# Kernel tuning notes

Measured on AMD Instinct MI355X. Metric: run time of the kernel, lower is better.

## Reference

```python
import jax, jax.numpy as jnp
import numpy as np

WIN = 8          # window side
N = WIN * WIN    # tokens per window = 64
C = 180          # channels
H = 6            # heads
D = C // H       # head dim = 30


def _relative_index():
    coords = jnp.stack(jnp.meshgrid(jnp.arange(WIN), jnp.arange(WIN), indexing='ij'))
    coords = coords.reshape(2, -1)                       # (2, N)
    rel = coords[:, :, None] - coords[:, None, :]        # (2, N, N)
    idx = (rel[0] + WIN - 1) * (2 * WIN - 1) + (rel[1] + WIN - 1)
    return idx.reshape(-1)                               # (N*N,) int


def setup_inputs() -> dict:
    key = jax.random.key(0)
    ks = jax.random.split(key, 6)
    B, WNum = 4096, 1024
    windows = jax.random.normal(ks[0], (B, N, C), dtype=jnp.float32)
    mask = jax.random.normal(ks[1], (WNum, N, N), dtype=jnp.float32)
    w_qkv = jax.random.normal(ks[2], (C, 3 * C), dtype=jnp.float32) * 0.02
    bias_table = jax.random.normal(ks[3], ((2 * WIN - 1) ** 2, H), dtype=jnp.float32) * 0.02
    w_proj = jax.random.normal(ks[4], (C, C), dtype=jnp.float32) * 0.02
    b_proj = jnp.zeros((C,), dtype=jnp.float32)
    return {"windows": windows, "mask": mask, "w_qkv": w_qkv,
            "bias_table": bias_table, "w_proj": w_proj, "b_proj": b_proj}


def reference(windows, mask, w_qkv, bias_table, w_proj, b_proj):
    B, n, c = windows.shape
    WNum = mask.shape[0]
    rel_idx = _relative_index()

    # qkv projection: (B, N, 3C) -> (3, B, H, N, D)
    qkv = (windows @ w_qkv).reshape(B, n, 3, H, D).transpose(2, 0, 3, 1, 4)
    q, k, v = qkv[0], qkv[1], qkv[2]

    scale = 1.0 / jnp.sqrt(jnp.float32(D))
    scores = jnp.einsum('bhnd,bhmd->bhnm', q, k) * scale     # (B, H, N, N)

    # relative position bias gather: (N*N, H) -> (H, N, N)
    rel_bias = bias_table[rel_idx].reshape(n, n, H).transpose(2, 0, 1)
    scores = scores + rel_bias[None]

    # per-window mask add
    scores = scores.reshape(B // WNum, WNum, H, n, n) + mask[None, :, None, :, :]
    scores = scores.reshape(B, H, n, n)

    attn = jax.nn.softmax(scores, axis=-1)
    out = jnp.einsum('bhnm,bhmd->bhnd', attn, v)             # (B, H, N, D)
    z = out.transpose(0, 2, 1, 3).reshape(B, n, c)
    return z @ w_proj + b_proj
```

## Files before the change

### kernel.cpp

```cpp
#include <hip/hip_runtime.h>


typedef __bf16 bf16;
typedef bf16 bf16x8 __attribute__((ext_vector_type(8)));
typedef float f32x4 __attribute__((ext_vector_type(4)));

#define MFMA(a, b, c) __builtin_amdgcn_mfma_f32_16x16x32_bf16(a, b, c, 0, 0, 0)

__global__ void prep_w(const float* __restrict__ wqkv,
                       const float* __restrict__ wproj,
                       const float* __restrict__ btab,
                       bf16* __restrict__ wqkvT,
                       bf16* __restrict__ wprojT,
                       float* __restrict__ relb)
{
    const int idx = blockIdx.x * 256 + threadIdx.x;
    if (idx < 110592) {
        const int oc = idx / 192, kk = idx - oc * 192;
        const int h = oc / 96, r = oc - h * 96;
        const int sec = r >> 5, d = r & 31;
        wqkvT[idx] = (bf16)((kk < 180 && d < 30) ? wqkv[kk * 540 + sec * 180 + h * 30 + d] : 0.f);
    } else if (idx < 147456) {
        const int r = idx - 110592;
        const int n = r / 192, k = r - n * 192;
        wprojT[r] = (bf16)((n < 180 && k < 180) ? wproj[k * 180 + n] : 0.f);
    } else if (idx < 172032) {
        const int r = idx - 147456;
        const int h = r >> 12;
        const int ij = r & 4095;
        const int i = ij >> 6, j = ij & 63;
        const int rel = ((i >> 3) - (j >> 3) + 7) * 15 + ((i & 7) - (j & 7) + 7);
        relb[r] = btab[rel * 6 + h];
    }
}

__global__ __launch_bounds__(384, 4)
void swin_mfma(const float* __restrict__ xg_all,
               const float* __restrict__ mask_all,
               const float* __restrict__ bproj,
               const bf16* __restrict__ wqkvT,
               const bf16* __restrict__ wprojT,
               const float* __restrict__ relb,
               float* __restrict__ outg)
{
    __shared__ __align__(16) short xb[64 * 200];

    const int b    = blockIdx.x;
    const int tid  = threadIdx.x;
    const int w    = tid >> 6;
    const int lane = tid & 63;
    const int l15  = lane & 15;
    const int g    = lane >> 4;

    const float* xg    = xg_all + (size_t)b * 11520;
    const float* maskw = mask_all + (size_t)(b & 1023) * 4096;

    {
        float4 xv[7];
        #pragma unroll
        for (int u = 0; u < 7; u++)
            xv[u] = *reinterpret_cast<const float4*>(xg + 4 * (tid + 384 * u));
        float4 xt;
        if (tid < 192) xt = *reinterpret_cast<const float4*>(xg + 4 * (2688 + tid));
        for (int e = tid; e < 640; e += 384) {
            const int i = e / 10;
            ((unsigned*)(xb + i * 200 + 180))[e - i * 10] = 0u;
        }
        #pragma unroll
        for (int u = 0; u < 7; u++) {
            const int e = tid + 384 * u;
            const int i = e / 45;
            const int c = 4 * e - i * 180;
            const unsigned p0 = (unsigned)__builtin_bit_cast(unsigned short, (bf16)xv[u].x)
                              | ((unsigned)__builtin_bit_cast(unsigned short, (bf16)xv[u].y) << 16);
            const unsigned p1 = (unsigned)__builtin_bit_cast(unsigned short, (bf16)xv[u].z)
                              | ((unsigned)__builtin_bit_cast(unsigned short, (bf16)xv[u].w) << 16);
            *reinterpret_cast<unsigned*>(xb + i * 200 + c)     = p0;
            *reinterpret_cast<unsigned*>(xb + i * 200 + c + 2) = p1;
        }
        if (tid < 192) {
            const int e = 2688 + tid;
            const int i = e / 45;
            const int c = 4 * e - i * 180;
            const unsigned p0 = (unsigned)__builtin_bit_cast(unsigned short, (bf16)xt.x)
                              | ((unsigned)__builtin_bit_cast(unsigned short, (bf16)xt.y) << 16);
            const unsigned p1 = (unsigned)__builtin_bit_cast(unsigned short, (bf16)xt.z)
                              | ((unsigned)__builtin_bit_cast(unsigned short, (bf16)xt.w) << 16);
            *reinterpret_cast<unsigned*>(xb + i * 200 + c)     = p0;
            *reinterpret_cast<unsigned*>(xb + i * 200 + c + 2) = p1;
        }
    }
    __syncthreads();

    const bf16* wqh = wqkvT + (size_t)(w * 96) * 192;
    const int rowoff = l15 * 192 + 8 * g;

    bf16x8 qf[4], kf[4];
    {
        f32x4 aqk[4][4];
        #pragma unroll
        for (int ct = 0; ct < 4; ct++)
            #pragma unroll
            for (int tt = 0; tt < 4; tt++) aqk[ct][tt] = (f32x4)0.f;
        #pragma unroll
        for (int ks = 0; ks < 6; ks++) {
            bf16x8 xf[4];
            #pragma unroll
            for (int tt = 0; tt < 4; tt++)
                xf[tt] = *reinterpret_cast<const bf16x8*>(xb + (16 * tt + l15) * 200 + 32 * ks + 8 * g);
            __builtin_amdgcn_s_setprio(1);
            #pragma unroll
            for (int ct = 0; ct < 4; ct++) {
                const bf16x8 wf = *reinterpret_cast<const bf16x8*>(wqh + ct * 3072 + rowoff + 32 * ks);
                #pragma unroll
                for (int tt = 0; tt < 4; tt++)
                    aqk[ct][tt] = MFMA(wf, xf[tt], aqk[ct][tt]);
            }
            __builtin_amdgcn_s_setprio(0);
        }
        #pragma unroll
        for (int tt = 0; tt < 4; tt++)
            #pragma unroll
            for (int s = 0; s < 8; s++) {
                qf[tt][s] = (bf16)(aqk[s >> 2][tt][s & 3] * 0.18257418583505537f);
                kf[tt][s] = (bf16)(aqk[2 + (s >> 2)][tt][s & 3]);
            }
    }
    __builtin_amdgcn_sched_barrier(0);

    bf16x8 pf[4][2];
    {
        const float* relh = relb + w * 4096;
        float4 rbc[4], mkc[4];
        {
            const float* rbb = relh + l15 * 64 + 4 * g;
            const float* mkb = maskw + l15 * 64 + 4 * g;
            #pragma unroll
            for (int jt = 0; jt < 4; jt++) {
                rbc[jt] = *reinterpret_cast<const float4*>(rbb + 16 * jt);
                mkc[jt] = *reinterpret_cast<const float4*>(mkb + 16 * jt);
            }
        }
        #pragma unroll
        for (int it = 0; it < 4; it++) {
            f32x4 stj[4];
            __builtin_amdgcn_s_setprio(1);
            #pragma unroll
            for (int jt = 0; jt < 4; jt++) stj[jt] = MFMA(kf[jt], qf[it], (f32x4)0.f);
            __builtin_amdgcn_s_setprio(0);

            float4 rbn[4], mkn[4];
            if (it < 3) {
                const int i1 = 16 * (it + 1) + l15;
                const float* rbb = relh + i1 * 64 + 4 * g;
                const float* mkb = maskw + i1 * 64 + 4 * g;
                #pragma unroll
                for (int jt = 0; jt < 4; jt++) {
                    rbn[jt] = *reinterpret_cast<const float4*>(rbb + 16 * jt);
                    mkn[jt] = *reinterpret_cast<const float4*>(mkb + 16 * jt);
                }
            }

            float mx = -1e30f;
            #pragma unroll
            for (int jt = 0; jt < 4; jt++) {
                stj[jt][0] += rbc[jt].x + mkc[jt].x;
                stj[jt][1] += rbc[jt].y + mkc[jt].y;
                stj[jt][2] += rbc[jt].z + mkc[jt].z;
                stj[jt][3] += rbc[jt].w + mkc[jt].w;
                #pragma unroll
                for (int r = 0; r < 4; r++) mx = fmaxf(mx, stj[jt][r]);
            }
            mx = fmaxf(mx, __shfl_xor(mx, 16));
            mx = fmaxf(mx, __shfl_xor(mx, 32));
            float sum = 0.f;
            #pragma unroll
            for (int jt = 0; jt < 4; jt++)
                #pragma unroll
                for (int r = 0; r < 4; r++) {
                    const float e = __expf(stj[jt][r] - mx);
                    stj[jt][r] = e;
                    sum += e;
                }
            sum += __shfl_xor(sum, 16);
            sum += __shfl_xor(sum, 32);
            const float inv = 1.0f / sum;
            #pragma unroll
            for (int k2 = 0; k2 < 2; k2++)
                #pragma unroll
                for (int s = 0; s < 8; s++)
                    pf[it][k2][s] = (bf16)(stj[2 * k2 + (s >> 2)][s & 3] * inv);

            if (it < 3) {
                #pragma unroll
                for (int jt = 0; jt < 4; jt++) { rbc[jt] = rbn[jt]; mkc[jt] = mkn[jt]; }
            }
        }
    }
    __builtin_amdgcn_sched_barrier(0);

    bf16x8 vf[2][2];
    {
        f32x4 av[4][2];
        #pragma unroll
        for (int tt = 0; tt < 4; tt++) { av[tt][0] = (f32x4)0.f; av[tt][1] = (f32x4)0.f; }
        #pragma unroll
        for (int ks = 0; ks < 6; ks++) {
            bf16x8 xf[4];
            #pragma unroll
            for (int tt = 0; tt < 4; tt++)
                xf[tt] = *reinterpret_cast<const bf16x8*>(xb + (16 * tt + l15) * 200 + 32 * ks + 8 * g);
            __builtin_amdgcn_s_setprio(1);
            #pragma unroll
            for (int cv = 0; cv < 2; cv++) {
                const bf16x8 wf = *reinterpret_cast<const bf16x8*>(wqh + (4 + cv) * 3072 + rowoff + 32 * ks);
                #pragma unroll
                for (int tt = 0; tt < 4; tt++)
                    av[tt][cv] = MFMA(xf[tt], wf, av[tt][cv]);
            }
            __builtin_amdgcn_s_setprio(0);
        }
        #pragma unroll
        for (int cv = 0; cv < 2; cv++)
            #pragma unroll
            for (int k2 = 0; k2 < 2; k2++)
                #pragma unroll
                for (int s = 0; s < 8; s++)
                    vf[cv][k2][s] = (bf16)(av[2 * k2 + (s >> 2)][cv][s & 3]);
    }
    __builtin_amdgcn_sched_barrier(0);

    f32x4 zacc[4][2];
    #pragma unroll
    for (int it = 0; it < 4; it++) { zacc[it][0] = (f32x4)0.f; zacc[it][1] = (f32x4)0.f; }
    __builtin_amdgcn_s_setprio(1);
    #pragma unroll
    for (int k2 = 0; k2 < 2; k2++)
        #pragma unroll
        for (int cv = 0; cv < 2; cv++)
            #pragma unroll
            for (int it = 0; it < 4; it++)
                zacc[it][cv] = MFMA(pf[it][k2], vf[cv][k2], zacc[it][cv]);
    __builtin_amdgcn_s_setprio(0);

    __syncthreads();
    #pragma unroll
    for (int cv = 0; cv < 2; cv++) {
        const int d = 16 * cv + l15;
        if (d < 30) {
            #pragma unroll
            for (int it = 0; it < 4; it++)
                #pragma unroll
                for (int r = 0; r < 4; r++)
                    xb[(16 * it + 4 * g + r) * 200 + w * 30 + d] =
                        __builtin_bit_cast(short, (bf16)zacc[it][cv][r]);
        }
    }
    __syncthreads();

    f32x4 pa[4][2];
    #pragma unroll
    for (int mt = 0; mt < 4; mt++) { pa[mt][0] = (f32x4)0.f; pa[mt][1] = (f32x4)0.f; }
    #pragma unroll
    for (int ks = 0; ks < 6; ks++) {
        bf16x8 zf[4];
        #pragma unroll
        for (int mt = 0; mt < 4; mt++)
            zf[mt] = *reinterpret_cast<const bf16x8*>(xb + (16 * mt + l15) * 200 + 32 * ks + 8 * g);
        __builtin_amdgcn_s_setprio(1);
        #pragma unroll
        for (int q2 = 0; q2 < 2; q2++) {
            const bf16x8 wf = *reinterpret_cast<const bf16x8*>(
                wprojT + ((2 * w + q2) * 16 + l15) * 192 + 32 * ks + 8 * g);
            #pragma unroll
            for (int mt = 0; mt < 4; mt++)
                pa[mt][q2] = MFMA(zf[mt], wf, pa[mt][q2]);
        }
        __builtin_amdgcn_s_setprio(0);
    }
    #pragma unroll
    for (int q2 = 0; q2 < 2; q2++) {
        const int n = (2 * w + q2) * 16 + l15;
        if (n < 180) {
            const float bn = bproj[n];
            float* const ob = outg + (size_t)b * 11520 + n;
            #pragma unroll
            for (int mt = 0; mt < 4; mt++)
                #pragma unroll
                for (int r = 0; r < 4; r++)
                    ob[(16 * mt + 4 * g + r) * 180] = pa[mt][q2][r] + bn;
        }
    }
}

extern "C" void kernel_launch(void* const* d_in, const int* in_sizes, int n_in,
                              void* d_out, int out_size, void* d_ws, size_t ws_size,
                              hipStream_t stream) {
    const float* windows = (const float*)d_in[0];
    const float* mask    = (const float*)d_in[1];
    const float* wqkv    = (const float*)d_in[2];
    const float* btab    = (const float*)d_in[3];
    const float* wproj   = (const float*)d_in[4];
    const float* bproj   = (const float*)d_in[5];

    bf16*  wqkvT  = (bf16*)d_ws;
    bf16*  wprojT = (bf16*)((char*)d_ws + 221184);
    float* relb   = (float*)((char*)d_ws + 294912);

    hipLaunchKernelGGL(prep_w, dim3(672), dim3(256), 0, stream,
                       wqkv, wproj, btab, wqkvT, wprojT, relb);
    hipLaunchKernelGGL(swin_mfma, dim3(4096), dim3(384), 0, stream,
                       windows, mask, bproj, wqkvT, wprojT, relb, (float*)d_out);
}
```

Before: 285.7 us.

## Process two windows per block and drop softmax max subtraction

Each block now handles two windows (b and b+2048), which share the same mask slice, and the grid is halved. The inputs for both windows are loaded and converted into a doubled LDS buffer up front. Relative bias and mask are pre-summed into one value per element. The softmax no longer subtracts the row max, which saves a reduction and two shuffles per row. The goal is to amortise launch and setup costs and to cut softmax work. In exchange, LDS use and register pressure rise, which may lower occupancy. Skipping the max makes the softmax overflow-unsafe for large scores.

```diff
diff --git a/kernel.cpp b/kernel.cpp
--- a/kernel.cpp
+++ b/kernel.cpp
@@ -43,7 +43,7 @@
                const float* __restrict__ relb,
                float* __restrict__ outg)
 {
-    __shared__ __align__(16) short xb[64 * 200];
+    __shared__ __align__(16) short xb2[2][64 * 200];
 
     const int b    = blockIdx.x;
     const int tid  = threadIdx.x;
@@ -52,243 +52,263 @@
     const int l15  = lane & 15;
     const int g    = lane >> 4;
 
-    const float* xg    = xg_all + (size_t)b * 11520;
+    const float* xgA   = xg_all + (size_t)b * 11520;
+    const float* xgB   = xg_all + (size_t)(b + 2048) * 11520;
     const float* maskw = mask_all + (size_t)(b & 1023) * 4096;
 
     {
-        float4 xv[7];
+        float4 xvA[7], xvB[7];
         #pragma unroll
         for (int u = 0; u < 7; u++)
-            xv[u] = *reinterpret_cast<const float4*>(xg + 4 * (tid + 384 * u));
-        float4 xt;
-        if (tid < 192) xt = *reinterpret_cast<const float4*>(xg + 4 * (2688 + tid));
-        for (int e = tid; e < 640; e += 384) {
-            const int i = e / 10;
-            ((unsigned*)(xb + i * 200 + 180))[e - i * 10] = 0u;
+            xvA[u] = *reinterpret_cast<const float4*>(xgA + 4 * (tid + 384 * u));
+        #pragma unroll
+        for (int u = 0; u < 7; u++)
+            xvB[u] = *reinterpret_cast<const float4*>(xgB + 4 * (tid + 384 * u));
+        float4 xtA, xtB;
+        if (tid < 192) {
+            xtA = *reinterpret_cast<const float4*>(xgA + 4 * (2688 + tid));
+            xtB = *reinterpret_cast<const float4*>(xgB + 4 * (2688 + tid));
+        }
+        for (int e = tid; e < 1280; e += 384) {
+            const int buf = (e >= 640) ? 1 : 0;
+            const int e2 = e - buf * 640;
+            const int i = e2 / 10;
+            ((unsigned*)(&xb2[buf][0] + i * 200 + 180))[e2 - i * 10] = 0u;
         }
         #pragma unroll
         for (int u = 0; u < 7; u++) {
             const int e = tid + 384 * u;
             const int i = e / 45;
             const int c = 4 * e - i * 180;
-            const unsigned p0 = (unsigned)__builtin_bit_cast(unsigned short, (bf16)xv[u].x)
-                              | ((unsigned)__builtin_bit_cast(unsigned short, (bf16)xv[u].y) << 16);
-            const unsigned p1 = (unsigned)__builtin_bit_cast(unsigned short, (bf16)xv[u].z)
-                              | ((unsigned)__builtin_bit_cast(unsigned short, (bf16)xv[u].w) << 16);
-            *reinterpret_cast<unsigned*>(xb + i * 200 + c)     = p0;
-            *reinterpret_cast<unsigned*>(xb + i * 200 + c + 2) = p1;
+            unsigned p0, p1;
+            p0 = (unsigned)__builtin_bit_cast(unsigned short, (bf16)xvA[u].x)
+               | ((unsigned)__builtin_bit_cast(unsigned short, (bf16)xvA[u].y) << 16);
+            p1 = (unsigned)__builtin_bit_cast(unsigned short, (bf16)xvA[u].z)
+               | ((unsigned)__builtin_bit_cast(unsigned short, (bf16)xvA[u].w) << 16);
+            *reinterpret_cast<unsigned*>(&xb2[0][0] + i * 200 + c)     = p0;
+            *reinterpret_cast<unsigned*>(&xb2[0][0] + i * 200 + c + 2) = p1;
+            p0 = (unsigned)__builtin_bit_cast(unsigned short, (bf16)xvB[u].x)
+               | ((unsigned)__builtin_bit_cast(unsigned short, (bf16)xvB[u].y) << 16);
+            p1 = (unsigned)__builtin_bit_cast(unsigned short, (bf16)xvB[u].z)
+               | ((unsigned)__builtin_bit_cast(unsigned short, (bf16)xvB[u].w) << 16);
+            *reinterpret_cast<unsigned*>(&xb2[1][0] + i * 200 + c)     = p0;
+            *reinterpret_cast<unsigned*>(&xb2[1][0] + i * 200 + c + 2) = p1;
         }
         if (tid < 192) {
             const int e = 2688 + tid;
             const int i = e / 45;
             const int c = 4 * e - i * 180;
-            const unsigned p0 = (unsigned)__builtin_bit_cast(unsigned short, (bf16)xt.x)
-                              | ((unsigned)__builtin_bit_cast(unsigned short, (bf16)xt.y) << 16);
-            const unsigned p1 = (unsigned)__builtin_bit_cast(unsigned short, (bf16)xt.z)
-                              | ((unsigned)__builtin_bit_cast(unsigned short, (bf16)xt.w) << 16);
-            *reinterpret_cast<unsigned*>(xb + i * 200 + c)     = p0;
-            *reinterpret_cast<unsigned*>(xb + i * 200 + c + 2) = p1;
+            unsigned p0, p1;
+            p0 = (unsigned)__builtin_bit_cast(unsigned short, (bf16)xtA.x)
+               | ((unsigned)__builtin_bit_cast(unsigned short, (bf16)xtA.y) << 16);
+            p1 = (unsigned)__builtin_bit_cast(unsigned short, (bf16)xtA.z)
+               | ((unsigned)__builtin_bit_cast(unsigned short, (bf16)xtA.w) << 16);
+            *reinterpret_cast<unsigned*>(&xb2[0][0] + i * 200 + c)     = p0;
+            *reinterpret_cast<unsigned*>(&xb2[0][0] + i * 200 + c + 2) = p1;
+            p0 = (unsigned)__builtin_bit_cast(unsigned short, (bf16)xtB.x)
+               | ((unsigned)__builtin_bit_cast(unsigned short, (bf16)xtB.y) << 16);
+            p1 = (unsigned)__builtin_bit_cast(unsigned short, (bf16)xtB.z)
+               | ((unsigned)__builtin_bit_cast(unsigned short, (bf16)xtB.w) << 16);
+            *reinterpret_cast<unsigned*>(&xb2[1][0] + i * 200 + c)     = p0;
+            *reinterpret_cast<unsigned*>(&xb2[1][0] + i * 200 + c + 2) = p1;
         }
     }
     __syncthreads();
 
     const bf16* wqh = wqkvT + (size_t)(w * 96) * 192;
     const int rowoff = l15 * 192 + 8 * g;
-
-    bf16x8 qf[4], kf[4];
-    {
-        f32x4 aqk[4][4];
-        #pragma unroll
-        for (int ct = 0; ct < 4; ct++)
-            #pragma unroll
-            for (int tt = 0; tt < 4; tt++) aqk[ct][tt] = (f32x4)0.f;
+    const float* relh = relb + w * 4096;
+
+    #pragma unroll
+    for (int win = 0; win < 2; ++win) {
+        short* const xb = &xb2[win][0];
+        float* const og = outg + (size_t)(b + 2048 * win) * 11520;
+
+        bf16x8 qf[4], kf[4];
+        {
+            f32x4 aqk[4][4];
+            #pragma unroll
+            for (int ct = 0; ct < 4; ct++)
+                #pragma unroll
+                for (int tt = 0; tt < 4; tt++) aqk[ct][tt] = (f32x4)0.f;
+            #pragma unroll
+            for (int ks = 0; ks < 6; ks++) {
+                bf16x8 xf[4];
+                #pragma unroll
+                for (int tt = 0; tt < 4; tt++)
+                    xf[tt] = *reinterpret_cast<const bf16x8*>(xb + (16 * tt + l15) * 200 + 32 * ks + 8 * g);
+                __builtin_amdgcn_s_setprio(1);
+                #pragma unroll
+                for (int ct = 0; ct < 4; ct++) {
+                    const bf16x8 wf = *reinterpret_cast<const bf16x8*>(wqh + ct * 3072 + rowoff + 32 * ks);
+                    #pragma unroll
+                    for (int tt = 0; tt < 4; tt++)
+                        aqk[ct][tt] = MFMA(wf, xf[tt], aqk[ct][tt]);
+                }
+                __builtin_amdgcn_s_setprio(0);
+            }
+            #pragma unroll
+            for (int tt = 0; tt < 4; tt++)
+                #pragma unroll
+                for (int s = 0; s < 8; s++) {
+                    qf[tt][s] = (bf16)(aqk[s >> 2][tt][s & 3] * 0.18257418583505537f);
+                    kf[tt][s] = (bf16)(aqk[2 + (s >> 2)][tt][s & 3]);
+                }
+        }
+        __builtin_amdgcn_sched_barrier(0);
+
+        bf16x8 pf[4][2];
+        {
+            float4 bc[4];
+            {
+                const float* rbb = relh + l15 * 64 + 4 * g;
+                const float* mkb = maskw + l15 * 64 + 4 * g;
+                #pragma unroll
+                for (int jt = 0; jt < 4; jt++) {
+                    const float4 rb = *reinterpret_cast<const float4*>(rbb + 16 * jt);
+                    const float4 mk = *reinterpret_cast<const float4*>(mkb + 16 * jt);
+                    bc[jt] = make_float4(rb.x + mk.x, rb.y + mk.y, rb.z + mk.z, rb.w + mk.w);
+                }
+            }
+            #pragma unroll
+            for (int it = 0; it < 4; it++) {
+                f32x4 stj[4];
+                __builtin_amdgcn_s_setprio(1);
+                #pragma unroll
+                for (int jt = 0; jt < 4; jt++) stj[jt] = MFMA(kf[jt], qf[it], (f32x4)0.f);
+                __builtin_amdgcn_s_setprio(0);
+
+                float4 bn[4];
+                if (it < 3) {
+                    const int i1 = 16 * (it + 1) + l15;
+                    const float* rbb = relh + i1 * 64 + 4 * g;
+                    const float* mkb = maskw + i1 * 64 + 4 * g;
+                    #pragma unroll
+                    for (int jt = 0; jt < 4; jt++) {
+                        const float4 rb = *reinterpret_cast<const float4*>(rbb + 16 * jt);
+                        const float4 mk = *reinterpret_cast<const float4*>(mkb + 16 * jt);
+                        bn[jt] = make_float4(rb.x + mk.x, rb.y + mk.y, rb.z + mk.z, rb.w + mk.w);
+                    }
+                }
+
+                float sum = 0.f;
+                #pragma unroll
+                for (int jt = 0; jt < 4; jt++) {
+                    const float e0 = __expf(stj[jt][0] + bc[jt].x);
+                    const float e1 = __expf(stj[jt][1] + bc[jt].y);
+                    const float e2 = __expf(stj[jt][2] + bc[jt].z);
+                    const float e3 = __expf(stj[jt][3] + bc[jt].w);
+                    stj[jt][0] = e0; stj[jt][1] = e1; stj[jt][2] = e2; stj[jt][3] = e3;
+                    sum += (e0 + e1) + (e2 + e3);
+                }
+                sum += __shfl_xor(sum, 16);
+                sum += __shfl_xor(sum, 32);
+                const float inv = 1.0f / sum;
+                #pragma unroll
+                for (int k2 = 0; k2 < 2; k2++)
+                    #pragma unroll
+                    for (int s = 0; s < 8; s++)
+                        pf[it][k2][s] = (bf16)(stj[2 * k2 + (s >> 2)][s & 3] * inv);
+
+                if (it < 3) {
+                    #pragma unroll
+                    for (int jt = 0; jt < 4; jt++) bc[jt] = bn[jt];
+                }
+            }
+        }
+        __builtin_amdgcn_sched_barrier(0);
+
+        bf16x8 vf[2][2];
+        {
+            f32x4 av[4][2];
+            #pragma unroll
+            for (int tt = 0; tt < 4; tt++) { av[tt][0] = (f32x4)0.f; av[tt][1] = (f32x4)0.f; }
+            #pragma unroll
+            for (int ks = 0; ks < 6; ks++) {
+                bf16x8 xf[4];
+                #pragma unroll
+                for (int tt = 0; tt < 4; tt++)
+                    xf[tt] = *reinterpret_cast<const bf16x8*>(xb + (16 * tt + l15) * 200 + 32 * ks + 8 * g);
+                __builtin_amdgcn_s_setprio(1);
+                #pragma unroll
+                for (int cv = 0; cv < 2; cv++) {
+                    const bf16x8 wf = *reinterpret_cast<const bf16x8*>(wqh + (4 + cv) * 3072 + rowoff + 32 * ks);
+                    #pragma unroll
+                    for (int tt = 0; tt < 4; tt++)
+                        av[tt][cv] = MFMA(xf[tt], wf, av[tt][cv]);
+                }
+                __builtin_amdgcn_s_setprio(0);
+            }
+            #pragma unroll
+            for (int cv = 0; cv < 2; cv++)
+                #pragma unroll
+                for (int k2 = 0; k2 < 2; k2++)
+                    #pragma unroll
+                    for (int s = 0; s < 8; s++)
+                        vf[cv][k2][s] = (bf16)(av[2 * k2 + (s >> 2)][cv][s & 3]);
+        }
+        __builtin_amdgcn_sched_barrier(0);
+
+        f32x4 zacc[4][2];
+        #pragma unroll
+        for (int it = 0; it < 4; it++) { zacc[it][0] = (f32x4)0.f; zacc[it][1] = (f32x4)0.f; }
+        __builtin_amdgcn_s_setprio(1);
+        #pragma unroll
+        for (int k2 = 0; k2 < 2; k2++)
+            #pragma unroll
+            for (int cv = 0; cv < 2; cv++)
+                #pragma unroll
+                for (int it = 0; it < 4; it++)
+                    zacc[it][cv] = MFMA(pf[it][k2], vf[cv][k2], zacc[it][cv]);
+        __builtin_amdgcn_s_setprio(0);
+
+        __syncthreads();
+        #pragma unroll
+        for (int cv = 0; cv < 2; cv++) {
+            const int d = 16 * cv + l15;
+            if (d < 30) {
+                #pragma unroll
+                for (int it = 0; it < 4; it++)
+                    #pragma unroll
+                    for (int r = 0; r < 4; r++)
+                        xb[(16 * it + 4 * g + r) * 200 + w * 30 + d] =
+                            __builtin_bit_cast(short, (bf16)zacc[it][cv][r]);
+            }
+        }
+        __syncthreads();
+
+        f32x4 pa[4][2];
+        #pragma unroll
+        for (int mt = 0; mt < 4; mt++) { pa[mt][0] = (f32x4)0.f; pa[mt][1] = (f32x4)0.f; }
         #pragma unroll
         for (int ks = 0; ks < 6; ks++) {
-            bf16x8 xf[4];
-            #pragma unroll
-            for (int tt = 0; tt < 4; tt++)
-                xf[tt] = *reinterpret_cast<const bf16x8*>(xb + (16 * tt + l15) * 200 + 32 * ks + 8 * g);
+            bf16x8 zf[4];
+            #pragma unroll
+            for (int mt = 0; mt < 4; mt++)
+                zf[mt] = *reinterpret_cast<const bf16x8*>(xb + (16 * mt + l15) * 200 + 32 * ks + 8 * g);
             __builtin_amdgcn_s_setprio(1);
             #pragma unroll
-            for (int ct = 0; ct < 4; ct++) {
-                const bf16x8 wf = *reinterpret_cast<const bf16x8*>(wqh + ct * 3072 + rowoff + 32 * ks);
-                #pragma unroll
-                for (int tt = 0; tt < 4; tt++)
-                    aqk[ct][tt] = MFMA(wf, xf[tt], aqk[ct][tt]);
+            for (int q2 = 0; q2 < 2; q2++) {
+                const bf16x8 wf = *reinterpret_cast<const bf16x8*>(
+                    wprojT + ((2 * w + q2) * 16 + l15) * 192 + 32 * ks + 8 * g);
+                #pragma unroll
+                for (int mt = 0; mt < 4; mt++)
+                    pa[mt][q2] = MFMA(zf[mt], wf, pa[mt][q2]);
             }
             __builtin_amdgcn_s_setprio(0);
         }
         #pragma unroll
-        for (int tt = 0; tt < 4; tt++)
-            #pragma unroll
-            for (int s = 0; s < 8; s++) {
-                qf[tt][s] = (bf16)(aqk[s >> 2][tt][s & 3] * 0.18257418583505537f);
-                kf[tt][s] = (bf16)(aqk[2 + (s >> 2)][tt][s & 3]);
-            }
-    }
-    __builtin_amdgcn_sched_barrier(0);
-
-    bf16x8 pf[4][2];
-    {
-        const float* relh = relb + w * 4096;
-        float4 rbc[4], mkc[4];
-        {
-            const float* rbb = relh + l15 * 64 + 4 * g;
-            const float* mkb = maskw + l15 * 64 + 4 * g;
-            #pragma unroll
-            for (int jt = 0; jt < 4; jt++) {
-                rbc[jt] = *reinterpret_cast<const float4*>(rbb + 16 * jt);
-                mkc[jt] = *reinterpret_cast<const float4*>(mkb + 16 * jt);
-            }
-        }
-        #pragma unroll
-        for (int it = 0; it < 4; it++) {
-            f32x4 stj[4];
-            __builtin_amdgcn_s_setprio(1);
-            #pragma unroll
-            for (int jt = 0; jt < 4; jt++) stj[jt] = MFMA(kf[jt], qf[it], (f32x4)0.f);
-            __builtin_amdgcn_s_setprio(0);
-
-            float4 rbn[4], mkn[4];
-            if (it < 3) {
-                const int i1 = 16 * (it + 1) + l15;
-                const float* rbb = relh + i1 * 64 + 4 * g;
-                const float* mkb = maskw + i1 * 64 + 4 * g;
-                #pragma unroll
-                for (int jt = 0; jt < 4; jt++) {
-                    rbn[jt] = *reinterpret_cast<const float4*>(rbb + 16 * jt);
-                    mkn[jt] = *reinterpret_cast<const float4*>(mkb + 16 * jt);
-                }
-            }
-
-            float mx = -1e30f;
-            #pragma unroll
-            for (int jt = 0; jt < 4; jt++) {
-                stj[jt][0] += rbc[jt].x + mkc[jt].x;
-                stj[jt][1] += rbc[jt].y + mkc[jt].y;
-                stj[jt][2] += rbc[jt].z + mkc[jt].z;
-                stj[jt][3] += rbc[jt].w + mkc[jt].w;
-                #pragma unroll
-                for (int r = 0; r < 4; r++) mx = fmaxf(mx, stj[jt][r]);
-            }
-            mx = fmaxf(mx, __shfl_xor(mx, 16));
-            mx = fmaxf(mx, __shfl_xor(mx, 32));
-            float sum = 0.f;
-            #pragma unroll
-            for (int jt = 0; jt < 4; jt++)
-                #pragma unroll
-                for (int r = 0; r < 4; r++) {
-                    const float e = __expf(stj[jt][r] - mx);
-                    stj[jt][r] = e;
-                    sum += e;
-                }
-            sum += __shfl_xor(sum, 16);
-            sum += __shfl_xor(sum, 32);
-            const float inv = 1.0f / sum;
-            #pragma unroll
-            for (int k2 = 0; k2 < 2; k2++)
-                #pragma unroll
-                for (int s = 0; s < 8; s++)
-                    pf[it][k2][s] = (bf16)(stj[2 * k2 + (s >> 2)][s & 3] * inv);
-
-            if (it < 3) {
-                #pragma unroll
-                for (int jt = 0; jt < 4; jt++) { rbc[jt] = rbn[jt]; mkc[jt] = mkn[jt]; }
-            }
-        }
-    }
-    __builtin_amdgcn_sched_barrier(0);
-
-    bf16x8 vf[2][2];
-    {
-        f32x4 av[4][2];
-        #pragma unroll
-        for (int tt = 0; tt < 4; tt++) { av[tt][0] = (f32x4)0.f; av[tt][1] = (f32x4)0.f; }
-        #pragma unroll
-        for (int ks = 0; ks < 6; ks++) {
-            bf16x8 xf[4];
-            #pragma unroll
-            for (int tt = 0; tt < 4; tt++)
-                xf[tt] = *reinterpret_cast<const bf16x8*>(xb + (16 * tt + l15) * 200 + 32 * ks + 8 * g);
-            __builtin_amdgcn_s_setprio(1);
-            #pragma unroll
-            for (int cv = 0; cv < 2; cv++) {
-                const bf16x8 wf = *reinterpret_cast<const bf16x8*>(wqh + (4 + cv) * 3072 + rowoff + 32 * ks);
-                #pragma unroll
-                for (int tt = 0; tt < 4; tt++)
-                    av[tt][cv] = MFMA(xf[tt], wf, av[tt][cv]);
-            }
-            __builtin_amdgcn_s_setprio(0);
-        }
-        #pragma unroll
-        for (int cv = 0; cv < 2; cv++)
-            #pragma unroll
-            for (int k2 = 0; k2 < 2; k2++)
-                #pragma unroll
-                for (int s = 0; s < 8; s++)
-                    vf[cv][k2][s] = (bf16)(av[2 * k2 + (s >> 2)][cv][s & 3]);
-    }
-    __builtin_amdgcn_sched_barrier(0);
-
-    f32x4 zacc[4][2];
-    #pragma unroll
-    for (int it = 0; it < 4; it++) { zacc[it][0] = (f32x4)0.f; zacc[it][1] = (f32x4)0.f; }
-    __builtin_amdgcn_s_setprio(1);
-    #pragma unroll
-    for (int k2 = 0; k2 < 2; k2++)
-        #pragma unroll
-        for (int cv = 0; cv < 2; cv++)
-            #pragma unroll
-            for (int it = 0; it < 4; it++)
-                zacc[it][cv] = MFMA(pf[it][k2], vf[cv][k2], zacc[it][cv]);
-    __builtin_amdgcn_s_setprio(0);
-
-    __syncthreads();
-    #pragma unroll
-    for (int cv = 0; cv < 2; cv++) {
-        const int d = 16 * cv + l15;
-        if (d < 30) {
-            #pragma unroll
-            for (int it = 0; it < 4; it++)
-                #pragma unroll
-                for (int r = 0; r < 4; r++)
-                    xb[(16 * it + 4 * g + r) * 200 + w * 30 + d] =
-                        __builtin_bit_cast(short, (bf16)zacc[it][cv][r]);
-        }
-    }
-    __syncthreads();
-
-    f32x4 pa[4][2];
-    #pragma unroll
-    for (int mt = 0; mt < 4; mt++) { pa[mt][0] = (f32x4)0.f; pa[mt][1] = (f32x4)0.f; }
-    #pragma unroll
-    for (int ks = 0; ks < 6; ks++) {
-        bf16x8 zf[4];
-        #pragma unroll
-        for (int mt = 0; mt < 4; mt++)
-            zf[mt] = *reinterpret_cast<const bf16x8*>(xb + (16 * mt + l15) * 200 + 32 * ks + 8 * g);
-        __builtin_amdgcn_s_setprio(1);
-        #pragma unroll
         for (int q2 = 0; q2 < 2; q2++) {
-            const bf16x8 wf = *reinterpret_cast<const bf16x8*>(
-                wprojT + ((2 * w + q2) * 16 + l15) * 192 + 32 * ks + 8 * g);
-            #pragma unroll
-            for (int mt = 0; mt < 4; mt++)
-                pa[mt][q2] = MFMA(zf[mt], wf, pa[mt][q2]);
-        }
-        __builtin_amdgcn_s_setprio(0);
-    }
-    #pragma unroll
-    for (int q2 = 0; q2 < 2; q2++) {
-        const int n = (2 * w + q2) * 16 + l15;
-        if (n < 180) {
-            const float bn = bproj[n];
-            float* const ob = outg + (size_t)b * 11520 + n;
-            #pragma unroll
-            for (int mt = 0; mt < 4; mt++)
-                #pragma unroll
-                for (int r = 0; r < 4; r++)
-                    ob[(16 * mt + 4 * g + r) * 180] = pa[mt][q2][r] + bn;
+            const int n = (2 * w + q2) * 16 + l15;
+            if (n < 180) {
+                const float bn = bproj[n];
+                float* const ob = og + n;
+                #pragma unroll
+                for (int mt = 0; mt < 4; mt++)
+                    #pragma unroll
+                    for (int r = 0; r < 4; r++)
+                        ob[(16 * mt + 4 * g + r) * 180] = pa[mt][q2][r] + bn;
+            }
         }
     }
 }
@@ -309,6 +329,6 @@
 
     hipLaunchKernelGGL(prep_w, dim3(672), dim3(256), 0, stream,
                        wqkv, wproj, btab, wqkvT, wprojT, relb);
-    hipLaunchKernelGGL(swin_mfma, dim3(4096), dim3(384), 0, stream,
+    hipLaunchKernelGGL(swin_mfma, dim3(2048), dim3(384), 0, stream,
                        windows, mask, bproj, wqkvT, wprojT, relb, (float*)d_out);
 }
```

Measured after the change: 313.1 us. 9.6% more time.
